# Optimization experiments

Measured on AMD Instinct MI355X. Metric: run time of the kernel, lower is better.

## Reference

```python
import jax, jax.numpy as jnp
import numpy as np

DIM = 768
N_HEADS = 12
HEAD_DIM = DIM // N_HEADS
HIDDEN = 4 * DIM
EPS = 1e-5


def _layernorm(x, g, b):
    m = jnp.mean(x, axis=-1, keepdims=True)
    v = jnp.mean(jnp.square(x - m), axis=-1, keepdims=True)
    return (x - m) * jax.lax.rsqrt(v + EPS) * g + b


def setup_inputs() -> dict:
    key = jax.random.key(0)
    ks = jax.random.split(key, 16)
    s = lambda fan_in: 1.0 / np.sqrt(fan_in)
    return {
        "x": jax.random.normal(ks[0], (2, 2048, DIM), dtype=jnp.float32),
        "ln1_g": jnp.ones((DIM,), jnp.float32),
        "ln1_b": jnp.zeros((DIM,), jnp.float32),
        "qkv_w": jax.random.uniform(ks[1], (DIM, 3 * DIM), jnp.float32, -s(DIM), s(DIM)),
        "qkv_b": jax.random.uniform(ks[2], (3 * DIM,), jnp.float32, -s(DIM), s(DIM)),
        "proj_w": jax.random.uniform(ks[3], (DIM, DIM), jnp.float32, -s(DIM), s(DIM)),
        "proj_b": jax.random.uniform(ks[4], (DIM,), jnp.float32, -s(DIM), s(DIM)),
        "ln2_g": jnp.ones((DIM,), jnp.float32),
        "ln2_b": jnp.zeros((DIM,), jnp.float32),
        "w1": jax.random.uniform(ks[5], (DIM, HIDDEN), jnp.float32, -s(DIM), s(DIM)),
        "b1": jax.random.uniform(ks[6], (HIDDEN,), jnp.float32, -s(DIM), s(DIM)),
        "w2": jax.random.uniform(ks[7], (HIDDEN, DIM), jnp.float32, -s(HIDDEN), s(HIDDEN)),
        "b2": jax.random.uniform(ks[8], (DIM,), jnp.float32, -s(HIDDEN), s(HIDDEN)),
    }


def reference(x, ln1_g, ln1_b, qkv_w, qkv_b, proj_w, proj_b, ln2_g, ln2_b, w1, b1, w2, b2):
    B, N, C = x.shape
    # ---- attention branch (pre-norm) ----
    h = _layernorm(x, ln1_g, ln1_b)
    qkv = (h @ qkv_w + qkv_b).reshape(B, N, 3, N_HEADS, HEAD_DIM)
    qkv = qkv.transpose(2, 0, 3, 1, 4)  # [3, B, H, N, Dh]
    q, k, v = qkv[0], qkv[1], qkv[2]
    scale = HEAD_DIM ** -0.5
    scores = jnp.einsum("bhnd,bhmd->bhnm", q, k) * scale  # [B,H,N,N]
    attn = jax.nn.softmax(scores, axis=-1)
    ctx = jnp.einsum("bhnm,bhmd->bhnd", attn, v)  # [B,H,N,Dh]
    ctx = ctx.transpose(0, 2, 1, 3).reshape(B, N, C)
    x = x + ctx @ proj_w + proj_b
    # ---- MLP branch (pre-norm) ----
    h = _layernorm(x, ln2_g, ln2_b)
    h = jax.nn.gelu(h @ w1 + b1, approximate=False)  # torch nn.GELU default = exact erf
    x = x + h @ w2 + b2
    return x
```

## Files before the change

### kernel.cpp

```cpp
#include <hip/hip_runtime.h>
#include <hip/hip_bf16.h>
#include <math.h>

#define DIM 768
#define NHEADS 12
#define HDIM 64
#define HIDDEN 3072
#define SEQ 2048
#define NTOK 4096
#define QKV3 2304

typedef __attribute__((ext_vector_type(8))) __bf16 bf16x8;
typedef __attribute__((ext_vector_type(4))) float f32x4;
typedef __attribute__((ext_vector_type(16))) float f32x16;

__device__ __forceinline__ ushort f32_bf16(float f) {
  union { float f; uint u; } c{f};
  uint u = c.u;
  u = (u + 0x7FFFu + ((u >> 16) & 1u)) >> 16;
  return (ushort)u;
}

__device__ __forceinline__ float bf16_f32(ushort u) {
  union { uint u; float f; } c{(uint)u << 16};
  return c.f;
}

__device__ __forceinline__ uint cvt_pk_bf16(float lo, float hi) {
  uint r;
  asm("v_cvt_pk_bf16_f32 %0, %1, %2" : "=v"(r) : "v"(lo), "v"(hi));
  return r;
}

#define EXP2F(x) __builtin_amdgcn_exp2f(x)

__device__ __forceinline__ void glds16(const ushort* g, ushort* l) {
  __builtin_amdgcn_global_load_lds(
      (const __attribute__((address_space(1))) unsigned int*)(const void*)g,
      (__attribute__((address_space(3))) unsigned int*)(void*)l, 16, 0, 0);
}

union U8 { uint u[4]; bf16x8 v; };

__global__ __launch_bounds__(256) void prep_kernel(
    const float* __restrict__ qkv_w, const float* __restrict__ proj_w,
    const float* __restrict__ w1, const float* __restrict__ w2,
    ushort* __restrict__ o0, ushort* __restrict__ o1,
    ushort* __restrict__ o2, ushort* __restrict__ o3,
    const float* __restrict__ x, const float* __restrict__ g1,
    const float* __restrict__ b1v, ushort* __restrict__ lnout) {
  int bid = blockIdx.x;
  int t = threadIdx.x;
  if (bid < 6912) {
    __shared__ float tile[32][33];
    const float* in; ushort* out; int K, N;
    if (bid < 1728)      { in = qkv_w;  out = o0; K = DIM;    N = QKV3; }
    else if (bid < 2304) { bid -= 1728; in = proj_w; out = o1; K = DIM;  N = DIM; }
    else if (bid < 4608) { bid -= 2304; in = w1;  out = o2; K = DIM;    N = HIDDEN; }
    else                 { bid -= 4608; in = w2;  out = o3; K = HIDDEN; N = DIM; }
    int ntx = N / 32;
    int nb = (bid % ntx) * 32, kb = (bid / ntx) * 32;
    int tx = t & 31, ty = t >> 5;
#pragma unroll
    for (int i = 0; i < 32; i += 8)
      tile[ty + i][tx] = in[(size_t)(kb + ty + i) * N + nb + tx];
    __syncthreads();
#pragma unroll
    for (int i = 0; i < 32; i += 8)
      out[(size_t)(nb + ty + i) * K + kb + tx] = f32_bf16(tile[tx][ty + i]);
  } else {
    int row = bid - 6912;
    const float* xr = x + (size_t)row * DIM;
    float v0 = xr[t], v1 = xr[t + 256], v2 = xr[t + 512];
    float s = v0 + v1 + v2;
    float q = v0 * v0 + v1 * v1 + v2 * v2;
#pragma unroll
    for (int m = 1; m < 64; m <<= 1) {
      s += __shfl_xor(s, m);
      q += __shfl_xor(q, m);
    }
    __shared__ float ss[4], qq[4];
    int wid = t >> 6;
    if ((t & 63) == 0) { ss[wid] = s; qq[wid] = q; }
    __syncthreads();
    s = ss[0] + ss[1] + ss[2] + ss[3];
    q = qq[0] + qq[1] + qq[2] + qq[3];
    float mean = s * (1.0f / DIM);
    float var = q * (1.0f / DIM) - mean * mean;
    float rs = rsqrtf(var + 1e-5f);
    size_t o = (size_t)row * DIM;
    lnout[o + t]       = f32_bf16((v0 - mean) * rs * g1[t]       + b1v[t]);
    lnout[o + t + 256] = f32_bf16((v1 - mean) * rs * g1[t + 256] + b1v[t + 256]);
    lnout[o + t + 512] = f32_bf16((v2 - mean) * rs * g1[t + 512] + b1v[t + 512]);
  }
}

__global__ __launch_bounds__(256) void ln_bf16(
    const float* __restrict__ x, const float* __restrict__ g,
    const float* __restrict__ bta, ushort* __restrict__ out) {
  int row = blockIdx.x;
  const float* xr = x + (size_t)row * DIM;
  int t = threadIdx.x;
  float v0 = xr[t], v1 = xr[t + 256], v2 = xr[t + 512];
  float s = v0 + v1 + v2;
  float q = v0 * v0 + v1 * v1 + v2 * v2;
#pragma unroll
  for (int m = 1; m < 64; m <<= 1) {
    s += __shfl_xor(s, m);
    q += __shfl_xor(q, m);
  }
  __shared__ float ss[4], qq[4];
  int wid = t >> 6;
  if ((t & 63) == 0) { ss[wid] = s; qq[wid] = q; }
  __syncthreads();
  s = ss[0] + ss[1] + ss[2] + ss[3];
  q = qq[0] + qq[1] + qq[2] + qq[3];
  float mean = s * (1.0f / DIM);
  float var = q * (1.0f / DIM) - mean * mean;
  float rs = rsqrtf(var + 1e-5f);
  size_t o = (size_t)row * DIM;
  out[o + t]       = f32_bf16((v0 - mean) * rs * g[t]       + bta[t]);
  out[o + t + 256] = f32_bf16((v1 - mean) * rs * g[t + 256] + bta[t + 256]);
  out[o + t + 512] = f32_bf16((v2 - mean) * rs * g[t + 512] + bta[t + 512]);
}

template <int EPI>
__global__ __launch_bounds__(256, 4) void gemm_bf16(
    const ushort* __restrict__ A, const ushort* __restrict__ Bt,
    const float* __restrict__ bias, const float* __restrict__ resid,
    void* __restrict__ outv, int M, int N, int K, int lda, int ldb,
    ushort* __restrict__ p0, ushort* __restrict__ p1, ushort* __restrict__ p2) {
  __shared__ __align__(16) ushort As[128 * 64];
  __shared__ __align__(16) ushort Bs[128 * 64];
  int t = threadIdx.x;
  int lane = t & 63, w = t >> 6;
  int wr = w >> 1, wc = w & 1;
  int nxy = gridDim.x * gridDim.y;
  int flat = blockIdx.x + gridDim.x * blockIdx.y;
  int swz = (flat & 7) * (nxy >> 3) + (flat >> 3);
  int m0 = (swz / gridDim.x) * 128, n0 = (swz % gridDim.x) * 128;
  int kb = blockIdx.z * K;
  f32x4 acc[4][4] = {};
  int rl = lane & 15, g = lane >> 4, rl7 = rl & 7;

  int baseRow = w * 32 + (lane >> 3);
  int cs = (lane & 7) ^ ((lane >> 3) & 7);
  const ushort* Asrc = A + (size_t)(m0 + baseRow) * lda + kb + cs * 8;
  const ushort* Bsrc = Bt + (size_t)(n0 + baseRow) * ldb + kb + cs * 8;
  ushort* Adst = &As[(w * 256 + lane) * 8];
  ushort* Bdst = &Bs[(w * 256 + lane) * 8];

  for (int k0 = 0; k0 < K; k0 += 64) {
    __syncthreads();
#pragma unroll
    for (int i = 0; i < 4; i++) {
      glds16(Asrc + (size_t)i * 8 * lda + k0, Adst + i * 512);
      glds16(Bsrc + (size_t)i * 8 * ldb + k0, Bdst + i * 512);
    }
    __syncthreads();
    bf16x8 a[2][4], b[2][4];
#pragma unroll
    for (int kk = 0; kk < 2; kk++)
#pragma unroll
      for (int i = 0; i < 4; i++) {
        a[kk][i] = *(const bf16x8*)&As[(wr * 64 + i * 16 + rl) * 64 + ((kk * 4 + g) ^ rl7) * 8];
        b[kk][i] = *(const bf16x8*)&Bs[(wc * 64 + i * 16 + rl) * 64 + ((kk * 4 + g) ^ rl7) * 8];
      }
#pragma unroll
    for (int kk = 0; kk < 2; kk++)
#pragma unroll
      for (int i = 0; i < 4; i++)
#pragma unroll
        for (int j = 0; j < 4; j++)
          acc[i][j] = __builtin_amdgcn_mfma_f32_16x16x32_bf16(a[kk][i], b[kk][j], acc[i][j], 0, 0, 0);
  }
  ushort* pz = (blockIdx.z == 0) ? p0 : ((blockIdx.z == 1) ? p1 : p2);
  int g4 = (lane >> 4) * 4;
#pragma unroll
  for (int i = 0; i < 4; i++) {
#pragma unroll
    for (int j = 0; j < 4; j++) {
      int col = n0 + wc * 64 + j * 16 + rl;
      float bval = (EPI == 3) ? 0.0f : bias[col];
#pragma unroll
      for (int r = 0; r < 4; r++) {
        int row = m0 + wr * 64 + i * 16 + g4 + r;
        float v = acc[i][j][r] + bval;
        if (EPI == 0) {
          ushort val = f32_bf16(v);
          if (col < 2 * DIM) {
            ((ushort*)outv)[(size_t)row * N + col] = val;
          } else {
            int hv = (col - 2 * DIM) >> 6, dd = (col - 2 * DIM) & 63;
            p0[((size_t)((row >> 11) * NHEADS + hv) * 64 + dd) * SEQ + (row & (SEQ - 1))] = val;
          }
        } else if (EPI == 1) {
          v += resid[(size_t)row * N + col];
          ((float*)outv)[(size_t)row * N + col] = v;
        } else if (EPI == 2) {
          v = 0.5f * v * (1.0f + erff(v * 0.70710678118654752f));
          ((ushort*)outv)[(size_t)row * N + col] = f32_bf16(v);
        } else {
          pz[(size_t)row * N + col] = f32_bf16(v);
        }
      }
    }
  }
}

__global__ __launch_bounds__(256) void reduce3_kernel(
    const ushort* __restrict__ p0, const ushort* __restrict__ p1,
    const ushort* __restrict__ p2, const float* __restrict__ x1,
    const float* __restrict__ bias, float* __restrict__ out) {
  int i = blockIdx.x * 256 + threadIdx.x;
  int col = (i * 4) % DIM;
  const ushort4 a0 = ((const ushort4*)p0)[i];
  const ushort4 a1 = ((const ushort4*)p1)[i];
  const ushort4 a2 = ((const ushort4*)p2)[i];
  const float4 xv = ((const float4*)x1)[i];
  const float4 bv = *(const float4*)&bias[col];
  float4 o;
  o.x = xv.x + bv.x + bf16_f32(a0.x) + bf16_f32(a1.x) + bf16_f32(a2.x);
  o.y = xv.y + bv.y + bf16_f32(a0.y) + bf16_f32(a1.y) + bf16_f32(a2.y);
  o.z = xv.z + bv.z + bf16_f32(a0.z) + bf16_f32(a1.z) + bf16_f32(a2.z);
  o.w = xv.w + bv.w + bf16_f32(a0.w) + bf16_f32(a1.w) + bf16_f32(a2.w);
  ((float4*)out)[i] = o;
}

__global__ __launch_bounds__(256, 3) void attn_kernel(
    const ushort* __restrict__ qkv, const ushort* __restrict__ vT,
    ushort* __restrict__ ctx) {
  __shared__ __align__(16) ushort Ks[128 * 64];
  __shared__ __align__(16) ushort Vt[64 * 128];
  __shared__ float mml[2][64];
  int t = threadIdx.x, lane = t & 63, w = t >> 6;
  int qh = w & 1, kvpar = w >> 1;
  int kl = lane & 31, hi = lane >> 5;
  int i0 = blockIdx.x;
  int xcd = i0 & 7, j = i0 >> 3;
  int qt = j & 31, grp = j >> 5;
  int pair = xcd + 8 * grp;
  int h = pair % 12, b = pair / 12;

  bf16x8 bq[4];
  {
    size_t qbase = (size_t)(b * SEQ + qt * 64 + qh * 32 + kl) * QKV3 + h * HDIM + hi * 8;
#pragma unroll
    for (int mi = 0; mi < 4; mi++) bq[mi] = *(const bf16x8*)(qkv + qbase + mi * 16);
#pragma unroll
    for (int mi = 0; mi < 4; mi++)
#pragma unroll
      for (int e = 0; e < 8; e++)
        bq[mi][e] = (__bf16)((float)bq[mi][e] * 0.18033688f);
  }
  f32x16 acc_o[2] = {};
  float lst = 0.0f;

  const ushort* kbase = qkv + (size_t)(b * SEQ) * QKV3 + DIM + h * HDIM;
  const ushort* vtb = vT + (size_t)(b * NHEADS + h) * 64 * SEQ;

  for (int kt = 0; kt < SEQ / 128; kt++) {
    __syncthreads();
#pragma unroll
    for (int i = 0; i < 4; i++) {
      int s = i * 256 + t;
      int krow = s >> 3, kcc = s & 7;
      glds16(kbase + (size_t)(kt * 128 + krow) * QKV3 + ((kcc ^ (krow & 7)) * 8),
             &Ks[s * 8]);
      int vrow = s >> 4, vcc = s & 15;
      glds16(vtb + (size_t)vrow * SEQ + kt * 128 + ((vcc ^ (vrow & 15)) * 8),
             &Vt[s * 8]);
    }
    __syncthreads();

    f32x16 accs[2] = {};
#pragma unroll
    for (int ks = 0; ks < 2; ks++) {
      int key = kvpar * 64 + ks * 32 + kl;
#pragma unroll
      for (int mi = 0; mi < 4; mi++) {
        bf16x8 ak = *(const bf16x8*)&Ks[key * 64 + (((2 * mi + hi) ^ (key & 7)) * 8)];
        accs[ks] = __builtin_amdgcn_mfma_f32_32x32x16_bf16(ak, bq[mi], accs[ks], 0, 0, 0);
      }
    }

    float ps = 0.0f;
    uint PK[2][8];
#pragma unroll
    for (int ks = 0; ks < 2; ks++)
#pragma unroll
      for (int rp = 0; rp < 8; rp++) {
        float p0 = EXP2F(accs[ks][2 * rp]);
        float p1 = EXP2F(accs[ks][2 * rp + 1]);
        ps += p0 + p1;
        PK[ks][rp] = cvt_pk_bf16(p0, p1);
      }
    ps += __shfl_xor(ps, 32);
    lst += ps;

#pragma unroll
    for (int tt = 0; tt < 4; tt++) {
      const int ks = tt >> 1, tb = 4 * (tt & 1);
      uint e0 = hi ? PK[ks][tb]     : PK[ks][tb + 2];
      uint e1 = hi ? PK[ks][tb + 1] : PK[ks][tb + 3];
      uint x0 = __shfl_xor(e0, 32), x1 = __shfl_xor(e1, 32);
      uint l0 = hi ? PK[ks][tb + 2] : PK[ks][tb];
      uint l1 = hi ? PK[ks][tb + 3] : PK[ks][tb + 1];
      U8 a;
      a.u[0] = hi ? x0 : l0;
      a.u[1] = hi ? x1 : l1;
      a.u[2] = hi ? l0 : x0;
      a.u[3] = hi ? l1 : x1;
      int chunk = kvpar * 8 + 2 * tt + hi;
#pragma unroll
      for (int dn = 0; dn < 2; dn++) {
        int d = dn * 32 + kl;
        bf16x8 bv = *(const bf16x8*)&Vt[d * 128 + ((chunk ^ (d & 15)) * 8)];
        acc_o[dn] = __builtin_amdgcn_mfma_f32_32x32x16_bf16(a.v, bv, acc_o[dn], 0, 0, 0);
      }
    }
  }

  __syncthreads();
  float* obuf = ((float*)Ks) + qh * 2048;
  if (kvpar == 1) {
#pragma unroll
    for (int dn = 0; dn < 2; dn++)
#pragma unroll
      for (int r = 0; r < 16; r++)
        obuf[(dn * 16 + r) * 64 + lane] = acc_o[dn][r];
    mml[qh][lane] = lst;
  }
  __syncthreads();
  if (kvpar == 0) {
    lst += mml[qh][lane];
    float inv = 1.0f / lst;
#pragma unroll
    for (int r = 0; r < 16; r++) {
      int qrow = (r & 3) + 8 * (r >> 2) + 4 * hi;
      int src = qrow | (lane & 32);
      float ir = __shfl(inv, src);
      size_t row = (size_t)(b * SEQ + qt * 64 + qh * 32 + qrow);
#pragma unroll
      for (int dn = 0; dn < 2; dn++) {
        float v = (acc_o[dn][r] + obuf[(dn * 16 + r) * 64 + lane]) * ir;
        ctx[row * DIM + h * HDIM + dn * 32 + kl] = f32_bf16(v);
      }
    }
  }
}

extern "C" void kernel_launch(void* const* d_in, const int* in_sizes, int n_in,
                              void* d_out, int out_size, void* d_ws, size_t ws_size,
                              hipStream_t stream) {
  const float* x      = (const float*)d_in[0];
  const float* ln1_g  = (const float*)d_in[1];
  const float* ln1_b  = (const float*)d_in[2];
  const float* qkv_w  = (const float*)d_in[3];
  const float* qkv_b  = (const float*)d_in[4];
  const float* proj_w = (const float*)d_in[5];
  const float* proj_b = (const float*)d_in[6];
  const float* ln2_g  = (const float*)d_in[7];
  const float* ln2_b  = (const float*)d_in[8];
  const float* w1     = (const float*)d_in[9];
  const float* b1     = (const float*)d_in[10];
  const float* w2     = (const float*)d_in[11];
  const float* b2     = (const float*)d_in[12];
  float* out = (float*)d_out;

  char* ws = (char*)d_ws;
  size_t off = 0;
  auto alloc = [&](size_t bytes) -> void* {
    void* p = ws + off;
    off += (bytes + 255) & ~(size_t)255;
    return p;
  };
  ushort* wqkv_t  = (ushort*)alloc((size_t)QKV3 * DIM * 2);
  ushort* wproj_t = (ushort*)alloc((size_t)DIM * DIM * 2);
  ushort* w1_t    = (ushort*)alloc((size_t)HIDDEN * DIM * 2);
  ushort* w2_t    = (ushort*)alloc((size_t)DIM * HIDDEN * 2);
  ushort* hbuf    = (ushort*)alloc((size_t)NTOK * DIM * 2);
  ushort* ubuf    = (ushort*)alloc((size_t)NTOK * HIDDEN * 2);
  ushort* ctx     = (ushort*)alloc((size_t)NTOK * DIM * 2);
  float*  x1      = (float*)alloc((size_t)NTOK * DIM * 4);
  ushort* qkvbuf = ubuf;
  ushort* m1     = ubuf;
  ushort* vT = (ushort*)x1;
  ushort* part0 = (ushort*)ws;
  ushort* part1 = hbuf;
  ushort* part2 = ctx;

  prep_kernel<<<6912 + NTOK, 256, 0, stream>>>(
      qkv_w, proj_w, w1, w2, wqkv_t, wproj_t, w1_t, w2_t,
      x, ln1_g, ln1_b, hbuf);

  gemm_bf16<0><<<dim3(QKV3 / 128, NTOK / 128), 256, 0, stream>>>(
      hbuf, wqkv_t, qkv_b, nullptr, qkvbuf, NTOK, QKV3, DIM, DIM, DIM,
      vT, nullptr, nullptr);
  attn_kernel<<<768, 256, 0, stream>>>(qkvbuf, vT, ctx);
  gemm_bf16<1><<<dim3(DIM / 128, NTOK / 128), 256, 0, stream>>>(
      ctx, wproj_t, proj_b, x, x1, NTOK, DIM, DIM, DIM, DIM,
      nullptr, nullptr, nullptr);
  ln_bf16<<<NTOK, 256, 0, stream>>>(x1, ln2_g, ln2_b, hbuf);
  gemm_bf16<2><<<dim3(HIDDEN / 128, NTOK / 128), 256, 0, stream>>>(
      hbuf, w1_t, b1, nullptr, m1, NTOK, HIDDEN, DIM, DIM, DIM,
      nullptr, nullptr, nullptr);
  gemm_bf16<3><<<dim3(DIM / 128, NTOK / 128, 3), 256, 0, stream>>>(
      m1, w2_t, nullptr, nullptr, nullptr, NTOK, DIM, HIDDEN / 3, HIDDEN, HIDDEN,
      part0, part1, part2);
  reduce3_kernel<<<NTOK * DIM / 4 / 256, 256, 0, stream>>>(
      part0, part1, part2, x1, b2, out);
}
```

Measured before the change: 180.7 us.

## Triple-buffer GEMM LDS tiles with async prefetch two stages ahead

After: 194.2 us. 1.08x slower.

```diff
diff --git a/kernel.cpp b/kernel.cpp
--- a/kernel.cpp
+++ b/kernel.cpp
@@ -125,55 +125,66 @@
 }
 
 template <int EPI>
-__global__ __launch_bounds__(256, 4) void gemm_bf16(
+__global__ __launch_bounds__(256, 3) void gemm_bf16(
     const ushort* __restrict__ A, const ushort* __restrict__ Bt,
     const float* __restrict__ bias, const float* __restrict__ resid,
     void* __restrict__ outv, int M, int N, int K, int lda, int ldb,
     ushort* __restrict__ p0, ushort* __restrict__ p1, ushort* __restrict__ p2) {
-  __shared__ __align__(16) ushort As[128 * 64];
-  __shared__ __align__(16) ushort Bs[128 * 64];
+  __shared__ __align__(16) ushort As[3][128 * 32];
+  __shared__ __align__(16) ushort Bs[3][128 * 32];
   int t = threadIdx.x;
   int lane = t & 63, w = t >> 6;
   int wr = w >> 1, wc = w & 1;
   int nxy = gridDim.x * gridDim.y;
   int flat = blockIdx.x + gridDim.x * blockIdx.y;
-  int swz = (flat & 7) * (nxy >> 3) + (flat >> 3);
-  int m0 = (swz / gridDim.x) * 128, n0 = (swz % gridDim.x) * 128;
+  int swzb = (flat & 7) * (nxy >> 3) + (flat >> 3);
+  int m0 = (swzb / gridDim.x) * 128, n0 = (swzb % gridDim.x) * 128;
   int kb = blockIdx.z * K;
   f32x4 acc[4][4] = {};
-  int rl = lane & 15, g = lane >> 4, rl7 = rl & 7;
-
-  int baseRow = w * 32 + (lane >> 3);
-  int cs = (lane & 7) ^ ((lane >> 3) & 7);
-  const ushort* Asrc = A + (size_t)(m0 + baseRow) * lda + kb + cs * 8;
-  const ushort* Bsrc = Bt + (size_t)(n0 + baseRow) * ldb + kb + cs * 8;
-  ushort* Adst = &As[(w * 256 + lane) * 8];
-  ushort* Bdst = &Bs[(w * 256 + lane) * 8];
-
-  for (int k0 = 0; k0 < K; k0 += 64) {
-    __syncthreads();
+  int rl = lane & 15, g = lane >> 4;
+
+  int r0 = t >> 2, c0 = (t & 3) ^ (r0 & 3);
+  int r1 = r0 + 64, c1 = (t & 3) ^ (r1 & 3);
+  const ushort* Asrc0 = A + (size_t)(m0 + r0) * lda + kb + c0 * 8;
+  const ushort* Bsrc0 = Bt + (size_t)(n0 + r0) * ldb + kb + c0 * 8;
+  const ushort* Asrc1 = A + (size_t)(m0 + r1) * lda + kb + c1 * 8;
+  const ushort* Bsrc1 = Bt + (size_t)(n0 + r1) * ldb + kb + c1 * 8;
+
+  const int nIt = K >> 5;
+  auto STAGE = [&](int tile, int stg) {
+    int k0 = tile << 5;
+    glds16(Asrc0 + k0, &As[stg][t * 8]);
+    glds16(Asrc1 + k0, &As[stg][(t + 256) * 8]);
+    glds16(Bsrc0 + k0, &Bs[stg][t * 8]);
+    glds16(Bsrc1 + k0, &Bs[stg][(t + 256) * 8]);
+  };
+  STAGE(0, 0);
+  STAGE(1, 1);
+  int sw = (g ^ (rl & 3)) * 8;
+
+  for (int it = 0; it < nIt; it++) {
+    int nx = it + 2;
+    STAGE(nx < nIt ? nx : nIt - 1, nx % 3);
+    asm volatile("s_waitcnt vmcnt(8)" ::: "memory");
+    __builtin_amdgcn_s_barrier();
+    asm volatile("" ::: "memory");
+    const ushort* AsB = As[it % 3];
+    const ushort* BsB = Bs[it % 3];
+    bf16x8 a[4], b[4];
 #pragma unroll
     for (int i = 0; i < 4; i++) {
-      glds16(Asrc + (size_t)i * 8 * lda + k0, Adst + i * 512);
-      glds16(Bsrc + (size_t)i * 8 * ldb + k0, Bdst + i * 512);
-    }
-    __syncthreads();
-    bf16x8 a[2][4], b[2][4];
-#pragma unroll
-    for (int kk = 0; kk < 2; kk++)
-#pragma unroll
-      for (int i = 0; i < 4; i++) {
-        a[kk][i] = *(const bf16x8*)&As[(wr * 64 + i * 16 + rl) * 64 + ((kk * 4 + g) ^ rl7) * 8];
-        b[kk][i] = *(const bf16x8*)&Bs[(wc * 64 + i * 16 + rl) * 64 + ((kk * 4 + g) ^ rl7) * 8];
-      }
-#pragma unroll
-    for (int kk = 0; kk < 2; kk++)
-#pragma unroll
-      for (int i = 0; i < 4; i++)
-#pragma unroll
-        for (int j = 0; j < 4; j++)
-          acc[i][j] = __builtin_amdgcn_mfma_f32_16x16x32_bf16(a[kk][i], b[kk][j], acc[i][j], 0, 0, 0);
-  }
+      a[i] = *(const bf16x8*)&AsB[(wr * 64 + i * 16 + rl) * 32 + sw];
+      b[i] = *(const bf16x8*)&BsB[(wc * 64 + i * 16 + rl) * 32 + sw];
+    }
+#pragma unroll
+    for (int i = 0; i < 4; i++)
+#pragma unroll
+      for (int j = 0; j < 4; j++)
+        acc[i][j] = __builtin_amdgcn_mfma_f32_16x16x32_bf16(a[i], b[j], acc[i][j], 0, 0, 0);
+    asm volatile("" ::: "memory");
+    __builtin_amdgcn_s_barrier();
+  }
+
   ushort* pz = (blockIdx.z == 0) ? p0 : ((blockIdx.z == 1) ? p1 : p2);
   int g4 = (lane >> 4) * 4;
 #pragma unroll
```

## Pre-pack K and V into MFMA fragment layout and load straight to registers

Applied to the files above, without the earlier changes.

Measured after the change: 205.7 us. 13.8% more time.

```diff
diff --git a/kernel.cpp b/kernel.cpp
--- a/kernel.cpp
+++ b/kernel.cpp
@@ -188,11 +188,20 @@
         float v = acc[i][j][r] + bval;
         if (EPI == 0) {
           ushort val = f32_bf16(v);
-          if (col < 2 * DIM) {
+          int p = row & (SEQ - 1), bb = row >> 11;
+          if (col < DIM) {
             ((ushort*)outv)[(size_t)row * N + col] = val;
+          } else if (col < 2 * DIM) {
+            int hv = (col - DIM) >> 6, dd = (col - DIM) & 63;
+            int bh = bb * NHEADS + hv;
+            int c = dd >> 3;
+            p0[((size_t)(bh * 64 + (p >> 5)) * 256 +
+                (c >> 1) * 64 + (c & 1) * 32 + (p & 31)) * 8 + (dd & 7)] = val;
           } else {
             int hv = (col - 2 * DIM) >> 6, dd = (col - 2 * DIM) & 63;
-            p0[((size_t)((row >> 11) * NHEADS + hv) * 64 + dd) * SEQ + (row & (SEQ - 1))] = val;
+            int bh = bb * NHEADS + hv;
+            p1[(((size_t)(bh * 16 + (p >> 7)) * 16 + ((p >> 3) & 15)) * 2 +
+                (dd >> 5)) * 256 + (dd & 31) * 8 + (p & 7)] = val;
           }
         } else if (EPI == 1) {
           v += resid[(size_t)row * N + col];
@@ -228,10 +237,9 @@
 }
 
 __global__ __launch_bounds__(256, 3) void attn_kernel(
-    const ushort* __restrict__ qkv, const ushort* __restrict__ vT,
-    ushort* __restrict__ ctx) {
-  __shared__ __align__(16) ushort Ks[128 * 64];
-  __shared__ __align__(16) ushort Vt[64 * 128];
+    const ushort* __restrict__ qkv, const ushort* __restrict__ Kp,
+    const ushort* __restrict__ Vp, ushort* __restrict__ ctx) {
+  __shared__ float obuf_s[2][2048];
   __shared__ float mml[2][64];
   int t = threadIdx.x, lane = t & 63, w = t >> 6;
   int qh = w & 1, kvpar = w >> 1;
@@ -241,6 +249,7 @@
   int qt = j & 31, grp = j >> 5;
   int pair = xcd + 8 * grp;
   int h = pair % 12, b = pair / 12;
+  int bh = b * NHEADS + h;
 
   bf16x8 bq[4];
   {
@@ -256,33 +265,32 @@
   f32x16 acc_o[2] = {};
   float lst = 0.0f;
 
-  const ushort* kbase = qkv + (size_t)(b * SEQ) * QKV3 + DIM + h * HDIM;
-  const ushort* vtb = vT + (size_t)(b * NHEADS + h) * 64 * SEQ;
+  const ushort* kp = Kp + (size_t)bh * 131072;
+  const ushort* vp = Vp + (size_t)bh * 131072;
+  int koff = (kvpar * 2) * 256 * 8 + (hi * 32 + kl) * 8;
+  int voff = ((kvpar * 8 + hi) * 2) * 256 + kl * 8;
 
   for (int kt = 0; kt < SEQ / 128; kt++) {
-    __syncthreads();
-#pragma unroll
-    for (int i = 0; i < 4; i++) {
-      int s = i * 256 + t;
-      int krow = s >> 3, kcc = s & 7;
-      glds16(kbase + (size_t)(kt * 128 + krow) * QKV3 + ((kcc ^ (krow & 7)) * 8),
-             &Ks[s * 8]);
-      int vrow = s >> 4, vcc = s & 15;
-      glds16(vtb + (size_t)vrow * SEQ + kt * 128 + ((vcc ^ (vrow & 15)) * 8),
-             &Vt[s * 8]);
-    }
-    __syncthreads();
+    bf16x8 kf[8];
+#pragma unroll
+    for (int ks = 0; ks < 2; ks++)
+#pragma unroll
+      for (int mi = 0; mi < 4; mi++)
+        kf[ks * 4 + mi] = *(const bf16x8*)&kp[(size_t)kt * 8192 + koff + ks * 2048 + mi * 512];
+    bf16x8 vf[8];
+#pragma unroll
+    for (int tt = 0; tt < 4; tt++)
+#pragma unroll
+      for (int dn = 0; dn < 2; dn++)
+        vf[tt * 2 + dn] = *(const bf16x8*)
+            &vp[(size_t)kt * 8192 + ((kvpar * 8 + 2 * tt + hi) * 2 + dn) * 256 + kl * 8];
 
     f32x16 accs[2] = {};
 #pragma unroll
-    for (int ks = 0; ks < 2; ks++) {
-      int key = kvpar * 64 + ks * 32 + kl;
-#pragma unroll
-      for (int mi = 0; mi < 4; mi++) {
-        bf16x8 ak = *(const bf16x8*)&Ks[key * 64 + (((2 * mi + hi) ^ (key & 7)) * 8)];
-        accs[ks] = __builtin_amdgcn_mfma_f32_32x32x16_bf16(ak, bq[mi], accs[ks], 0, 0, 0);
-      }
-    }
+    for (int ks = 0; ks < 2; ks++)
+#pragma unroll
+      for (int mi = 0; mi < 4; mi++)
+        accs[ks] = __builtin_amdgcn_mfma_f32_32x32x16_bf16(kf[ks * 4 + mi], bq[mi], accs[ks], 0, 0, 0);
 
     float ps = 0.0f;
     uint PK[2][8];
@@ -311,18 +319,14 @@
       a.u[1] = hi ? x1 : l1;
       a.u[2] = hi ? l0 : x0;
       a.u[3] = hi ? l1 : x1;
-      int chunk = kvpar * 8 + 2 * tt + hi;
-#pragma unroll
-      for (int dn = 0; dn < 2; dn++) {
-        int d = dn * 32 + kl;
-        bf16x8 bv = *(const bf16x8*)&Vt[d * 128 + ((chunk ^ (d & 15)) * 8)];
-        acc_o[dn] = __builtin_amdgcn_mfma_f32_32x32x16_bf16(a.v, bv, acc_o[dn], 0, 0, 0);
-      }
+#pragma unroll
+      for (int dn = 0; dn < 2; dn++)
+        acc_o[dn] = __builtin_amdgcn_mfma_f32_32x32x16_bf16(a.v, vf[tt * 2 + dn], acc_o[dn], 0, 0, 0);
     }
   }
 
   __syncthreads();
-  float* obuf = ((float*)Ks) + qh * 2048;
+  float* obuf = obuf_s[qh];
   if (kvpar == 1) {
 #pragma unroll
     for (int dn = 0; dn < 2; dn++)
@@ -385,7 +389,8 @@
   float*  x1      = (float*)alloc((size_t)NTOK * DIM * 4);
   ushort* qkvbuf = ubuf;
   ushort* m1     = ubuf;
-  ushort* vT = (ushort*)x1;
+  ushort* Kp = (ushort*)x1;
+  ushort* Vp = (ushort*)x1 + (size_t)NTOK * DIM;
   ushort* part0 = (ushort*)ws;
   ushort* part1 = hbuf;
   ushort* part2 = ctx;
@@ -396,8 +401,8 @@
 
   gemm_bf16<0><<<dim3(QKV3 / 128, NTOK / 128), 256, 0, stream>>>(
       hbuf, wqkv_t, qkv_b, nullptr, qkvbuf, NTOK, QKV3, DIM, DIM, DIM,
-      vT, nullptr, nullptr);
-  attn_kernel<<<768, 256, 0, stream>>>(qkvbuf, vT, ctx);
+      Kp, Vp, nullptr);
+  attn_kernel<<<768, 256, 0, stream>>>(qkvbuf, Kp, Vp, ctx);
   gemm_bf16<1><<<dim3(DIM / 128, NTOK / 128), 256, 0, stream>>>(
       ctx, wproj_t, proj_b, x, x1, NTOK, DIM, DIM, DIM, DIM,
       nullptr, nullptr, nullptr);
```

## Split-K the projection GEMM and fuse partial reduction with residual and LayerNorm

Applied to the files above, without the earlier changes.

New measurement: 179.7 us. No clear change (-0.6%).

```diff
diff --git a/kernel.cpp b/kernel.cpp
--- a/kernel.cpp
+++ b/kernel.cpp
@@ -93,35 +93,6 @@
     lnout[o + t + 256] = f32_bf16((v1 - mean) * rs * g1[t + 256] + b1v[t + 256]);
     lnout[o + t + 512] = f32_bf16((v2 - mean) * rs * g1[t + 512] + b1v[t + 512]);
   }
-}
-
-__global__ __launch_bounds__(256) void ln_bf16(
-    const float* __restrict__ x, const float* __restrict__ g,
-    const float* __restrict__ bta, ushort* __restrict__ out) {
-  int row = blockIdx.x;
-  const float* xr = x + (size_t)row * DIM;
-  int t = threadIdx.x;
-  float v0 = xr[t], v1 = xr[t + 256], v2 = xr[t + 512];
-  float s = v0 + v1 + v2;
-  float q = v0 * v0 + v1 * v1 + v2 * v2;
-#pragma unroll
-  for (int m = 1; m < 64; m <<= 1) {
-    s += __shfl_xor(s, m);
-    q += __shfl_xor(q, m);
-  }
-  __shared__ float ss[4], qq[4];
-  int wid = t >> 6;
-  if ((t & 63) == 0) { ss[wid] = s; qq[wid] = q; }
-  __syncthreads();
-  s = ss[0] + ss[1] + ss[2] + ss[3];
-  q = qq[0] + qq[1] + qq[2] + qq[3];
-  float mean = s * (1.0f / DIM);
-  float var = q * (1.0f / DIM) - mean * mean;
-  float rs = rsqrtf(var + 1e-5f);
-  size_t o = (size_t)row * DIM;
-  out[o + t]       = f32_bf16((v0 - mean) * rs * g[t]       + bta[t]);
-  out[o + t + 256] = f32_bf16((v1 - mean) * rs * g[t + 256] + bta[t + 256]);
-  out[o + t + 512] = f32_bf16((v2 - mean) * rs * g[t + 512] + bta[t + 512]);
 }
 
 template <int EPI>
@@ -208,6 +179,48 @@
   }
 }
 
+__global__ __launch_bounds__(256) void reduceLN_kernel(
+    const ushort* __restrict__ p0, const ushort* __restrict__ p1,
+    const ushort* __restrict__ p2, const float* __restrict__ x,
+    const float* __restrict__ bias, const float* __restrict__ g,
+    const float* __restrict__ bta, float* __restrict__ x1,
+    ushort* __restrict__ lnout) {
+  int row = blockIdx.x;
+  int t = threadIdx.x;
+  size_t base = (size_t)row * DIM;
+  float v[3];
+  float s = 0.0f, q = 0.0f;
+#pragma unroll
+  for (int e = 0; e < 3; e++) {
+    int col = t + e * 256;
+    size_t idx = base + col;
+    float val = x[idx] + bias[col] + bf16_f32(p0[idx]) + bf16_f32(p1[idx]) + bf16_f32(p2[idx]);
+    x1[idx] = val;
+    v[e] = val;
+    s += val;
+    q += val * val;
+  }
+#pragma unroll
+  for (int m = 1; m < 64; m <<= 1) {
+    s += __shfl_xor(s, m);
+    q += __shfl_xor(q, m);
+  }
+  __shared__ float ss[4], qq[4];
+  int wid = t >> 6;
+  if ((t & 63) == 0) { ss[wid] = s; qq[wid] = q; }
+  __syncthreads();
+  s = ss[0] + ss[1] + ss[2] + ss[3];
+  q = qq[0] + qq[1] + qq[2] + qq[3];
+  float mean = s * (1.0f / DIM);
+  float var = q * (1.0f / DIM) - mean * mean;
+  float rs = rsqrtf(var + 1e-5f);
+#pragma unroll
+  for (int e = 0; e < 3; e++) {
+    int col = t + e * 256;
+    lnout[base + col] = f32_bf16((v[e] - mean) * rs * g[col] + bta[col]);
+  }
+}
+
 __global__ __launch_bounds__(256) void reduce3_kernel(
     const ushort* __restrict__ p0, const ushort* __restrict__ p1,
     const ushort* __restrict__ p2, const float* __restrict__ x1,
@@ -386,6 +399,9 @@
   ushort* qkvbuf = ubuf;
   ushort* m1     = ubuf;
   ushort* vT = (ushort*)x1;
+  ushort* pp0 = ubuf;
+  ushort* pp1 = ubuf + (size_t)NTOK * DIM;
+  ushort* pp2 = ubuf + (size_t)2 * NTOK * DIM;
   ushort* part0 = (ushort*)ws;
   ushort* part1 = hbuf;
   ushort* part2 = ctx;
@@ -398,10 +414,11 @@
       hbuf, wqkv_t, qkv_b, nullptr, qkvbuf, NTOK, QKV3, DIM, DIM, DIM,
       vT, nullptr, nullptr);
   attn_kernel<<<768, 256, 0, stream>>>(qkvbuf, vT, ctx);
-  gemm_bf16<1><<<dim3(DIM / 128, NTOK / 128), 256, 0, stream>>>(
-      ctx, wproj_t, proj_b, x, x1, NTOK, DIM, DIM, DIM, DIM,
-      nullptr, nullptr, nullptr);
-  ln_bf16<<<NTOK, 256, 0, stream>>>(x1, ln2_g, ln2_b, hbuf);
+  gemm_bf16<3><<<dim3(DIM / 128, NTOK / 128, 3), 256, 0, stream>>>(
+      ctx, wproj_t, nullptr, nullptr, nullptr, NTOK, DIM, DIM / 3, DIM, DIM,
+      pp0, pp1, pp2);
+  reduceLN_kernel<<<NTOK, 256, 0, stream>>>(
+      pp0, pp1, pp2, x, proj_b, ln2_g, ln2_b, x1, hbuf);
   gemm_bf16<2><<<dim3(HIDDEN / 128, NTOK / 128), 256, 0, stream>>>(
       hbuf, w1_t, b1, nullptr, m1, NTOK, HIDDEN, DIM, DIM, DIM,
       nullptr, nullptr, nullptr);
```
